# Performance work log

Measured on AMD Instinct MI355X. Metric: run time of the kernel, lower is better.

Reference implementation:

```python
import jax, jax.numpy as jnp
import numpy as np

N = 8192        # batch of embeddings
D = 128         # embedding dim
NUM_STEPS = 201 # histogram bins over [-1, 1]


def setup_inputs() -> dict:
    key = jax.random.key(0)
    k1, k2, k3, k4 = jax.random.split(key, 4)
    x1 = jax.random.normal(k1, (N, D), dtype=jnp.float32)
    x2 = jax.random.normal(k2, (N, D), dtype=jnp.float32)
    # module assumes L2-normalized embeddings (cosine similarity via plain mm)
    x1 = x1 / jnp.linalg.norm(x1, axis=1, keepdims=True)
    x2 = x2 / jnp.linalg.norm(x2, axis=1, keepdims=True)
    t1 = jax.random.normal(k3, (N,), dtype=jnp.float32)
    t2 = jax.random.normal(k4, (N,), dtype=jnp.float32)
    return {"input_1": x1, "input_2": x2, "target_1": t1, "target_2": t2}


def reference(input_1, input_2, target_1, target_2):
    num_steps = NUM_STEPS
    step = 2.0 / (num_steps - 1)
    n = input_1.shape[0]

    # pairwise cosine similarities [N, N]
    sims = jnp.matmul(input_1, input_2.T)

    # pair signs: signs[i, j] = target_2[i] * target_1[j] > 0 (as in source layout)
    signs = (target_2[:, None] * target_1[None, :]) > 0.0
    triu = jnp.triu(jnp.ones((n, n), dtype=bool), 1)  # strictly upper pairs
    pos_mask = (triu & signs).reshape(-1)
    neg_mask = (triu & ~signs).reshape(-1)

    s = sims.reshape(-1)
    # triangular-kernel soft binning: lower bin edge delta = floor((s+1)/step)*step - 1
    idx = jnp.clip(jnp.floor((s + 1.0) / step).astype(jnp.int32), 0, num_steps - 1)
    delta = idx.astype(s.dtype) * step - 1.0
    frac = (s - delta) / step              # weight for upper bin (idx+1)
    idx_hi = jnp.clip(idx + 1, 0, num_steps - 1)

    def soft_hist(mask):
        w = mask.astype(s.dtype)
        h = jnp.zeros((num_steps,), dtype=s.dtype)
        h = h.at[idx].add((1.0 - frac) * w)   # lower-bin weight
        h = h.at[idx_hi].add(frac * w)        # upper-bin weight
        return h / jnp.maximum(w.sum(), 1.0)

    h_pos = soft_hist(pos_mask)
    h_neg = soft_hist(neg_mask)

    # CDF of positive histogram; loss = E[neg overlaps pos-CDF]
    pos_cdf = jnp.cumsum(h_pos)
    return jnp.sum(h_neg * pos_cdf)
```

## Files before the change

kernel.cpp:

```cpp
#include <hip/hip_runtime.h>

#define N_EMB   8192
#define D_EMB   128
#define NSTEPS  201
#define NB      128
#define TBLOCKS (NB*(NB+1)/2)
#define NCOPY   16
#define NHIST   16
#define PGRID   1536

typedef __attribute__((ext_vector_type(8))) short bf16x8;
typedef __attribute__((ext_vector_type(4))) float f32x4;

#define CNT_SHIFT  21
#define FRAC_MASK  ((1u << CNT_SHIFT) - 1u)
#define NZERO      (NCOPY * 2 * NSTEPS)

__device__ __forceinline__ unsigned short f2bf(float f) {
  unsigned int u = __builtin_bit_cast(unsigned int, f);
  u = (u + 0x7fffu + ((u >> 16) & 1u)) >> 16;
  return (unsigned short)u;
}

__device__ __forceinline__ void tile_coords(int t, int& bi, int& bj) {
  int rem = TBLOCKS - 1 - t;
  int r   = (int)((sqrtf(8.0f*(float)rem + 1.0f) - 1.0f) * 0.5f);
  while ((r+1)*(r+2)/2 <= rem) ++r;
  while (r*(r+1)/2 > rem) --r;
  bi = NB - 1 - r;
  bj = NB - 1 - (rem - r*(r+1)/2);
}

__global__ __launch_bounds__(256) void convert_kernel(
    const float* __restrict__ x1, const float* __restrict__ x2,
    unsigned short* __restrict__ x1b, unsigned short* __restrict__ x2b,
    float* __restrict__ ghist)
{
  int t = blockIdx.x * 256 + threadIdx.x;
  if (t < NZERO) ghist[t] = 0.0f;
  const float*    src = (t < 131072) ? x1  : x2;
  unsigned short* dst = (t < 131072) ? x1b : x2b;
  int tt  = t & 131071;
  int r   = tt >> 4;
  int c16 = tt & 15;
  const float4* g = reinterpret_cast<const float4*>(src + ((size_t)r << 7) + c16*8);
  float4 v0 = g[0], v1 = g[1];
  int R = r >> 4, fr = r & 15, K = c16 >> 2, kg = c16 & 3;
  size_t chunk = ((size_t)(R*4 + K) << 6) + (size_t)(kg*16 + fr);
  uint4 p;
  p.x = f2bf(v0.x) | ((unsigned int)f2bf(v0.y) << 16);
  p.y = f2bf(v0.z) | ((unsigned int)f2bf(v0.w) << 16);
  p.z = f2bf(v1.x) | ((unsigned int)f2bf(v1.y) << 16);
  p.w = f2bf(v1.z) | ((unsigned int)f2bf(v1.w) << 16);
  *reinterpret_cast<uint4*>(dst + chunk*8) = p;
}

__global__ __launch_bounds__(256, 6) void main_kernel(
    const unsigned short* __restrict__ x1b, const unsigned short* __restrict__ x2b,
    const float* __restrict__ t1g, const float* __restrict__ t2g,
    float* __restrict__ ghist)
{
  __shared__ unsigned int whist[2][NHIST][NSTEPS];

  const int tid = threadIdx.x;
  for (int b = tid; b < 2*NHIST*NSTEPS; b += 256) ((unsigned int*)whist)[b] = 0u;

  const int lane = tid & 63;
  const int w    = tid >> 6;
  const int wr   = w >> 1, wc = w & 1;
  const int fr   = lane & 15;
  const int kg   = lane >> 4;
  const int rbase = kg * 4;
  unsigned int* whP = &whist[0][(w << 2) | kg][0];
  const int NEGOFF = NHIST * NSTEPS;

  const int t0  = (int)(((long)blockIdx.x       * TBLOCKS) / PGRID);
  const int t1e = (int)(((long)(blockIdx.x + 1) * TBLOCKS) / PGRID);

  __syncthreads();

  for (int t = t0; t < t1e; ++t) {
    int bi, bj; tile_coords(t, bi, bj);
    const int gi0 = bi*64, gj0 = bj*64;
    const bool full = (bi != bj);

    const int Ra = (gi0 >> 4) + wr*2;
    const int Rb = (gj0 >> 4) + wc*2;
    f32x4 acc00 = {0.f,0.f,0.f,0.f}, acc01 = {0.f,0.f,0.f,0.f};
    f32x4 acc10 = {0.f,0.f,0.f,0.f}, acc11 = {0.f,0.f,0.f,0.f};
#pragma unroll
    for (int ks = 0; ks < 4; ++ks) {
      bf16x8 a0 = *reinterpret_cast<const bf16x8*>(x1b + ((((size_t)Ra    *4 + ks)*64 + lane) << 3));
      bf16x8 a1 = *reinterpret_cast<const bf16x8*>(x1b + ((((size_t)(Ra+1)*4 + ks)*64 + lane) << 3));
      bf16x8 b0 = *reinterpret_cast<const bf16x8*>(x2b + ((((size_t)Rb    *4 + ks)*64 + lane) << 3));
      bf16x8 b1 = *reinterpret_cast<const bf16x8*>(x2b + ((((size_t)(Rb+1)*4 + ks)*64 + lane) << 3));
      acc00 = __builtin_amdgcn_mfma_f32_16x16x32_bf16(a0, b0, acc00, 0, 0, 0);
      acc01 = __builtin_amdgcn_mfma_f32_16x16x32_bf16(a0, b1, acc01, 0, 0, 0);
      acc10 = __builtin_amdgcn_mfma_f32_16x16x32_bf16(a1, b0, acc10, 0, 0, 0);
      acc11 = __builtin_amdgcn_mfma_f32_16x16x32_bf16(a1, b1, acc11, 0, 0, 0);
    }

    float T2v[2][4], T1v[2];
#pragma unroll
    for (int tm = 0; tm < 2; ++tm)
#pragma unroll
      for (int rr = 0; rr < 4; ++rr) T2v[tm][rr] = t2g[gi0 + wr*32 + tm*16 + rbase + rr];
    T1v[0] = t1g[gj0 + wc*32 + fr];
    T1v[1] = t1g[gj0 + wc*32 + 16 + fr];

    auto dep = [&](const f32x4& a, int tm, int tn) {
      const int lj = wc*32 + tn*16 + fr;
      const float t1v = T1v[tn];
#pragma unroll
      for (int rr = 0; rr < 4; ++rr) {
        const int li = wr*32 + tm*16 + rbase + rr;
        bool pos = (T2v[tm][rr] * t1v > 0.0f);
        float uu = fmaf(a[rr], 102400.0f, 102400.5f);
        int   iu = (int)uu;
        int  idx = iu >> 10;
        idx = idx < 0 ? 0 : (idx > NSTEPS-1 ? NSTEPS-1 : idx);
        unsigned int pk = (1u << CNT_SHIFT) | (unsigned int)(iu & 1023);
        unsigned int* dst = whP + (pos ? 0 : NEGOFF) + idx;
        if (full || (lj > li)) atomicAdd(dst, pk);
      }
    };
    dep(acc00, 0, 0); dep(acc01, 0, 1);
    dep(acc10, 1, 0); dep(acc11, 1, 1);
  }
  __syncthreads();

  float* gh = ghist + (size_t)(blockIdx.x & (NCOPY-1)) * (2*NSTEPS);
  if (tid < NSTEPS) {
    const int b = tid;
    const float inv = 1.0f / 1024.0f;
#pragma unroll
    for (int sg = 0; sg < 2; ++sg) {
      unsigned int cp = 0; float fp = 0.f, fpm1 = 0.f;
#pragma unroll
      for (int ww = 0; ww < NHIST; ++ww) {
        unsigned int vp = whist[sg][ww][b];
        cp += vp >> CNT_SHIFT;  fp += (float)(vp & FRAC_MASK);
        if (b > 0) fpm1 += (float)(whist[sg][ww][b-1] & FRAC_MASK);
      }
      float hv = (b == NSTEPS-1) ? ((float)cp + fpm1 * inv)
                                 : ((float)cp - fp * inv + fpm1 * inv);
      if (hv != 0.0f) atomicAdd(&gh[sg*NSTEPS + b], hv);
    }
  }
}

__global__ void finalize_kernel(const float* __restrict__ ghist,
                                float* __restrict__ out)
{
  __shared__ float hp[NSTEPS], hn[NSTEPS];
  const int tid = threadIdx.x;
  if (tid < NSTEPS) {
    float sp = 0.f, sn = 0.f;
#pragma unroll
    for (int c = 0; c < NCOPY; ++c) {
      sp += ghist[(size_t)c*(2*NSTEPS) + tid];
      sn += ghist[(size_t)c*(2*NSTEPS) + NSTEPS + tid];
    }
    hp[tid] = sp; hn[tid] = sn;
  }
  __syncthreads();
  if (tid == 0) {
    const float TOT = 33550336.0f;
    float np = 0.f;
    for (int b = 0; b < NSTEPS; ++b) np += hp[b];
    float nn = TOT - np;
    float ip = 1.0f / fmaxf(np, 1.0f);
    float in_ = 1.0f / fmaxf(nn, 1.0f);
    float cdf = 0.f, loss = 0.f;
    for (int b = 0; b < NSTEPS; ++b) {
      cdf  += hp[b] * ip;
      loss += hn[b] * in_ * cdf;
    }
    out[0] = loss;
  }
}

extern "C" void kernel_launch(void* const* d_in, const int* in_sizes, int n_in,
                              void* d_out, int out_size, void* d_ws, size_t ws_size,
                              hipStream_t stream) {
  const float* x1 = (const float*)d_in[0];
  const float* x2 = (const float*)d_in[1];
  const float* t1 = (const float*)d_in[2];
  const float* t2 = (const float*)d_in[3];
  float* out = (float*)d_out;

  const size_t BF_BYTES = (size_t)N_EMB * D_EMB * sizeof(unsigned short);
  char* p = (char*)d_ws;
  unsigned short* x1b   = (unsigned short*)p;   p += BF_BYTES;
  unsigned short* x2b   = (unsigned short*)p;   p += BF_BYTES;
  float*          ghist = (float*)p;

  convert_kernel<<<(2*N_EMB*D_EMB/8 + 255)/256, 256, 0, stream>>>(x1, x2, x1b, x2b, ghist);
  main_kernel<<<PGRID, 256, 0, stream>>>(x1b, x2b, t1, t2, ghist);
  finalize_kernel<<<1, 256, 0, stream>>>(ghist, out);
}
```

Before: 47.73 us.

## Use 128x128 tiles with one tile per block and fuse finalize via last-block

Each block now computes a single 128x128 upper-triangular tile, with each wave holding a 4x4 grid of MFMA accumulators. This replaces the old loop over 64x64 tiles spread across a fixed persistent grid and gives more operand reuse per load. The separate finalize kernel is removed: a global done-counter lets the last block to finish reduce the histograms and compute the loss, saving one kernel launch. In exchange, register pressure rises (launch bounds lowered to 4 blocks per SM), diagonal tiles waste more work, and the grid shrinks to 2080 blocks.

```diff
diff --git a/kernel.cpp b/kernel.cpp
--- a/kernel.cpp
+++ b/kernel.cpp
@@ -3,11 +3,10 @@
 #define N_EMB   8192
 #define D_EMB   128
 #define NSTEPS  201
-#define NB      128
+#define NB      64
 #define TBLOCKS (NB*(NB+1)/2)
 #define NCOPY   16
 #define NHIST   16
-#define PGRID   1536
 
 typedef __attribute__((ext_vector_type(8))) short bf16x8;
 typedef __attribute__((ext_vector_type(4))) float f32x4;
@@ -34,10 +33,11 @@
 __global__ __launch_bounds__(256) void convert_kernel(
     const float* __restrict__ x1, const float* __restrict__ x2,
     unsigned short* __restrict__ x1b, unsigned short* __restrict__ x2b,
-    float* __restrict__ ghist)
+    float* __restrict__ ghist, unsigned int* __restrict__ gdone)
 {
   int t = blockIdx.x * 256 + threadIdx.x;
   if (t < NZERO) ghist[t] = 0.0f;
+  else if (t == NZERO) gdone[0] = 0u;
   const float*    src = (t < 131072) ? x1  : x2;
   unsigned short* dst = (t < 131072) ? x1b : x2b;
   int tt  = t & 131071;
@@ -55,12 +55,15 @@
   *reinterpret_cast<uint4*>(dst + chunk*8) = p;
 }
 
-__global__ __launch_bounds__(256, 6) void main_kernel(
+__global__ __launch_bounds__(256, 4) void main_kernel(
     const unsigned short* __restrict__ x1b, const unsigned short* __restrict__ x2b,
     const float* __restrict__ t1g, const float* __restrict__ t2g,
-    float* __restrict__ ghist)
+    float* __restrict__ ghist, unsigned int* __restrict__ gdone,
+    float* __restrict__ out)
 {
   __shared__ unsigned int whist[2][NHIST][NSTEPS];
+  __shared__ float hfin[2][NSTEPS];
+  __shared__ int lastFlag;
 
   const int tid = threadIdx.x;
   for (int b = tid; b < 2*NHIST*NSTEPS; b += 256) ((unsigned int*)whist)[b] = 0u;
@@ -74,48 +77,55 @@
   unsigned int* whP = &whist[0][(w << 2) | kg][0];
   const int NEGOFF = NHIST * NSTEPS;
 
-  const int t0  = (int)(((long)blockIdx.x       * TBLOCKS) / PGRID);
-  const int t1e = (int)(((long)(blockIdx.x + 1) * TBLOCKS) / PGRID);
+  int bi, bj; tile_coords((int)blockIdx.x, bi, bj);
+  const int gi0 = bi*128, gj0 = bj*128;
+  const bool full = (bi != bj);
+
+  const int Ra = (gi0 >> 4) + wr*4;
+  const int Rb = (gj0 >> 4) + wc*4;
 
   __syncthreads();
 
-  for (int t = t0; t < t1e; ++t) {
-    int bi, bj; tile_coords(t, bi, bj);
-    const int gi0 = bi*64, gj0 = bj*64;
-    const bool full = (bi != bj);
-
-    const int Ra = (gi0 >> 4) + wr*2;
-    const int Rb = (gj0 >> 4) + wc*2;
-    f32x4 acc00 = {0.f,0.f,0.f,0.f}, acc01 = {0.f,0.f,0.f,0.f};
-    f32x4 acc10 = {0.f,0.f,0.f,0.f}, acc11 = {0.f,0.f,0.f,0.f};
-#pragma unroll
-    for (int ks = 0; ks < 4; ++ks) {
-      bf16x8 a0 = *reinterpret_cast<const bf16x8*>(x1b + ((((size_t)Ra    *4 + ks)*64 + lane) << 3));
-      bf16x8 a1 = *reinterpret_cast<const bf16x8*>(x1b + ((((size_t)(Ra+1)*4 + ks)*64 + lane) << 3));
-      bf16x8 b0 = *reinterpret_cast<const bf16x8*>(x2b + ((((size_t)Rb    *4 + ks)*64 + lane) << 3));
-      bf16x8 b1 = *reinterpret_cast<const bf16x8*>(x2b + ((((size_t)(Rb+1)*4 + ks)*64 + lane) << 3));
-      acc00 = __builtin_amdgcn_mfma_f32_16x16x32_bf16(a0, b0, acc00, 0, 0, 0);
-      acc01 = __builtin_amdgcn_mfma_f32_16x16x32_bf16(a0, b1, acc01, 0, 0, 0);
-      acc10 = __builtin_amdgcn_mfma_f32_16x16x32_bf16(a1, b0, acc10, 0, 0, 0);
-      acc11 = __builtin_amdgcn_mfma_f32_16x16x32_bf16(a1, b1, acc11, 0, 0, 0);
-    }
-
-    float T2v[2][4], T1v[2];
-#pragma unroll
-    for (int tm = 0; tm < 2; ++tm)
-#pragma unroll
-      for (int rr = 0; rr < 4; ++rr) T2v[tm][rr] = t2g[gi0 + wr*32 + tm*16 + rbase + rr];
-    T1v[0] = t1g[gj0 + wc*32 + fr];
-    T1v[1] = t1g[gj0 + wc*32 + 16 + fr];
-
-    auto dep = [&](const f32x4& a, int tm, int tn) {
-      const int lj = wc*32 + tn*16 + fr;
-      const float t1v = T1v[tn];
+  f32x4 acc[4][4];
+#pragma unroll
+  for (int m = 0; m < 4; ++m)
+#pragma unroll
+    for (int n = 0; n < 4; ++n) acc[m][n] = f32x4{0.f,0.f,0.f,0.f};
+
+#pragma unroll
+  for (int ks = 0; ks < 4; ++ks) {
+    bf16x8 af[4], bf[4];
+#pragma unroll
+    for (int q = 0; q < 4; ++q) {
+      af[q] = *reinterpret_cast<const bf16x8*>(x1b + ((((size_t)(Ra+q)*4 + ks)*64 + lane) << 3));
+      bf[q] = *reinterpret_cast<const bf16x8*>(x2b + ((((size_t)(Rb+q)*4 + ks)*64 + lane) << 3));
+    }
+#pragma unroll
+    for (int m = 0; m < 4; ++m)
+#pragma unroll
+      for (int n = 0; n < 4; ++n)
+        acc[m][n] = __builtin_amdgcn_mfma_f32_16x16x32_bf16(af[m], bf[n], acc[m][n], 0, 0, 0);
+  }
+
+  float T2v[4][4], T1v[4];
+#pragma unroll
+  for (int m = 0; m < 4; ++m)
+#pragma unroll
+    for (int rr = 0; rr < 4; ++rr) T2v[m][rr] = t2g[gi0 + wr*64 + m*16 + rbase + rr];
+#pragma unroll
+  for (int n = 0; n < 4; ++n) T1v[n] = t1g[gj0 + wc*64 + n*16 + fr];
+
+#pragma unroll
+  for (int m = 0; m < 4; ++m) {
+#pragma unroll
+    for (int n = 0; n < 4; ++n) {
+      const int lj = wc*64 + n*16 + fr;
+      const float t1v = T1v[n];
 #pragma unroll
       for (int rr = 0; rr < 4; ++rr) {
-        const int li = wr*32 + tm*16 + rbase + rr;
-        bool pos = (T2v[tm][rr] * t1v > 0.0f);
-        float uu = fmaf(a[rr], 102400.0f, 102400.5f);
+        const int li = wr*64 + m*16 + rbase + rr;
+        bool pos = (T2v[m][rr] * t1v > 0.0f);
+        float uu = fmaf(acc[m][n][rr], 102400.0f, 102400.5f);
         int   iu = (int)uu;
         int  idx = iu >> 10;
         idx = idx < 0 ? 0 : (idx > NSTEPS-1 ? NSTEPS-1 : idx);
@@ -123,9 +133,7 @@
         unsigned int* dst = whP + (pos ? 0 : NEGOFF) + idx;
         if (full || (lj > li)) atomicAdd(dst, pk);
       }
-    };
-    dep(acc00, 0, 0); dep(acc01, 0, 1);
-    dep(acc10, 1, 0); dep(acc11, 1, 1);
+    }
   }
   __syncthreads();
 
@@ -147,36 +155,40 @@
       if (hv != 0.0f) atomicAdd(&gh[sg*NSTEPS + b], hv);
     }
   }
-}
-
-__global__ void finalize_kernel(const float* __restrict__ ghist,
-                                float* __restrict__ out)
-{
-  __shared__ float hp[NSTEPS], hn[NSTEPS];
-  const int tid = threadIdx.x;
-  if (tid < NSTEPS) {
-    float sp = 0.f, sn = 0.f;
-#pragma unroll
-    for (int c = 0; c < NCOPY; ++c) {
-      sp += ghist[(size_t)c*(2*NSTEPS) + tid];
-      sn += ghist[(size_t)c*(2*NSTEPS) + NSTEPS + tid];
-    }
-    hp[tid] = sp; hn[tid] = sn;
+
+  if (tid == 0) {
+    __threadfence();
+    unsigned int prev = atomicAdd(gdone, 1u);
+    lastFlag = (prev == (unsigned int)(TBLOCKS - 1));
   }
   __syncthreads();
-  if (tid == 0) {
-    const float TOT = 33550336.0f;
-    float np = 0.f;
-    for (int b = 0; b < NSTEPS; ++b) np += hp[b];
-    float nn = TOT - np;
-    float ip = 1.0f / fmaxf(np, 1.0f);
-    float in_ = 1.0f / fmaxf(nn, 1.0f);
-    float cdf = 0.f, loss = 0.f;
-    for (int b = 0; b < NSTEPS; ++b) {
-      cdf  += hp[b] * ip;
-      loss += hn[b] * in_ * cdf;
-    }
-    out[0] = loss;
+  if (lastFlag) {
+    __threadfence();
+    if (tid < NSTEPS) {
+      float sp = 0.f, sn = 0.f;
+      const volatile float* gv = ghist;
+#pragma unroll
+      for (int c = 0; c < NCOPY; ++c) {
+        sp += gv[(size_t)c*(2*NSTEPS) + tid];
+        sn += gv[(size_t)c*(2*NSTEPS) + NSTEPS + tid];
+      }
+      hfin[0][tid] = sp; hfin[1][tid] = sn;
+    }
+    __syncthreads();
+    if (tid == 0) {
+      const float TOT = 33550336.0f;
+      float np = 0.f;
+      for (int b = 0; b < NSTEPS; ++b) np += hfin[0][b];
+      float nn = TOT - np;
+      float ip  = 1.0f / fmaxf(np, 1.0f);
+      float in_ = 1.0f / fmaxf(nn, 1.0f);
+      float cdf = 0.f, loss = 0.f;
+      for (int b = 0; b < NSTEPS; ++b) {
+        cdf  += hfin[0][b] * ip;
+        loss += hfin[1][b] * in_ * cdf;
+      }
+      out[0] = loss;
+    }
   }
 }
 
@@ -193,9 +205,9 @@
   char* p = (char*)d_ws;
   unsigned short* x1b   = (unsigned short*)p;   p += BF_BYTES;
   unsigned short* x2b   = (unsigned short*)p;   p += BF_BYTES;
-  float*          ghist = (float*)p;
-
-  convert_kernel<<<(2*N_EMB*D_EMB/8 + 255)/256, 256, 0, stream>>>(x1, x2, x1b, x2b, ghist);
-  main_kernel<<<PGRID, 256, 0, stream>>>(x1b, x2b, t1, t2, ghist);
-  finalize_kernel<<<1, 256, 0, stream>>>(ghist, out);
-}
+  float*          ghist = (float*)p;            p += (size_t)NZERO*sizeof(float);
+  unsigned int*   gdone = (unsigned int*)p;
+
+  convert_kernel<<<(2*N_EMB*D_EMB/8 + 255)/256, 256, 0, stream>>>(x1, x2, x1b, x2b, ghist, gdone);
+  main_kernel<<<TBLOCKS, 256, 0, stream>>>(x1b, x2b, t1, t2, ghist, gdone, out);
+}
```

Result: slower. 90.90 us (+90.5%).
